# Optimization experiments

Measured on AMD Instinct MI355X. Metric: run time of the kernel, lower is better.

Reference implementation:

```python
import jax, jax.numpy as jnp
import numpy as np

B = 1024        # number of dialogs
MX_LEN = 110    # max utterances per dialog (alpha width hardcoded to 110 in source)
G_DIM = 512     # node feature dim
WP, WF = 10, 10 # past / future window
ALPHA_W = 110
NEG = -1e9


def setup_inputs() -> dict:
    key = jax.random.key(0)
    k1, k2, k3 = jax.random.split(key, 3)
    node_features = jax.random.normal(k1, (B, MX_LEN, G_DIM), dtype=jnp.float32)
    var = 2.0 / (G_DIM + G_DIM)  # matches torch init: normal_(0, var)
    weight = jax.random.normal(k2, (G_DIM, G_DIM), dtype=jnp.float32) * var
    text_len = jax.random.randint(k3, (B,), 1, MX_LEN + 1)
    return {"node_features": node_features, "weight": weight, "text_len": text_len}


def reference(node_features, weight, text_len):
    Bsz, L, D = node_features.shape
    # att_matrix[b, l] = weight @ node_features[b, l]
    att = jnp.einsum('de,ble->bld', weight, node_features)            # [B, L, D]
    # score[b, j, l] = att[b, l] . node_features[b, j]
    scores = jnp.einsum('bld,bjd->bjl', att, node_features)           # [B, J, Lkey]
    j = jnp.arange(L)[:, None]   # query position
    l = jnp.arange(L)[None, :]   # key position
    lens = text_len[:, None, None]                                    # [B, 1, 1]
    # window: s = max(0, j-wp), e = min(j+wf, cur_len-1); valid only for j < cur_len
    mask = (l >= j - WP) & (l <= j + WF) & (l <= lens - 1) & (j <= lens - 1)
    probs = jax.nn.softmax(jnp.where(mask, scores, NEG), axis=-1)
    probs = jnp.where(mask, probs, 0.0)                               # [B, L, L]
    # alpha is [mx_len, 110] per batch, zero outside window; stack over batch
    alpha = jnp.zeros((Bsz, L, ALPHA_W), dtype=probs.dtype).at[:, :, :L].set(probs)
    return alpha
```

## Files before the change

kernel.cpp:

```cpp
#include <hip/hip_runtime.h>
#include <stdint.h>

#define L_SZ 110
#define D_SZ 512
#define OUT_W 110
#define A_STRIDE 520
#define C_STRIDE 136
#define A_ROWS 112
#define ATT_ROWS 112
#define NF_ROWS 112
#define G3_ST 40

typedef __attribute__((ext_vector_type(8))) __bf16 bf16x8;
typedef __attribute__((ext_vector_type(4))) __bf16 bf16x4;
typedef __attribute__((ext_vector_type(4))) float f32x4;

__global__ __launch_bounds__(256) void wconv_kernel(const float* __restrict__ W,
                                                    __bf16* __restrict__ wbf) {
    int idx = blockIdx.x * 256 + threadIdx.x;
    float4 w = ((const float4*)W)[idx];
    bf16x4 o;
    o[0] = (__bf16)w.x; o[1] = (__bf16)w.y; o[2] = (__bf16)w.z; o[3] = (__bf16)w.w;
    ((bf16x4*)wbf)[idx] = o;
}

__global__ __launch_bounds__(256, 5) void att_gemm6_kernel(
    const float* __restrict__ nf, const __bf16* __restrict__ wbf,
    const int* __restrict__ tlenp, __bf16* __restrict__ attws,
    __bf16* __restrict__ nfbf)
{
    __shared__ __bf16 A_lds[64 * G3_ST];
    __shared__ __bf16 B_lds[128 * G3_ST];

    const int b   = blockIdx.y;
    const int cg  = blockIdx.x & 3;
    const int mh  = blockIdx.x >> 2;
    const int tid = threadIdx.x;
    const int lane = tid & 63;
    const int wave = tid >> 6;
    const int l15  = lane & 15;
    const int quad = lane >> 4;

    int len = tlenp[b];
    if (len > L_SZ) len = L_SZ;
    if (len < 1) len = 1;
    const int T = (len + 15) >> 4;
    if (T <= mh * 4) return;
    const int Tl = (T - mh * 4 < 4) ? (T - mh * 4) : 4;
    const int rows_needed = T << 4;
    const int rbase = mh << 6;

    const float* nfb = nf + (size_t)b * (L_SZ * D_SZ);

    const int r0 = tid >> 2;
    const int c8 = (tid & 3) << 3;
    const int ga = rbase + r0;
    const int astat = (ga >= rows_needed) ? 0 : ((ga < L_SZ) ? 1 : 2);

    f32x4 acc[4][2];
    const f32x4 fz = {0.f, 0.f, 0.f, 0.f};
    #pragma unroll
    for (int m = 0; m < 4; ++m) { acc[m][0] = fz; acc[m][1] = fz; }

    float4 abuf[2];
    bf16x8 bbuf[2];

    auto load_tiles = [&](int k0) {
        if (astat == 1) {
            const float* ap = nfb + (size_t)ga * D_SZ + k0 + c8;
            abuf[0] = *(const float4*)ap;
            abuf[1] = *(const float4*)(ap + 4);
        }
        #pragma unroll
        for (int s = 0; s < 2; ++s)
            bbuf[s] = *(const bf16x8*)&wbf[(size_t)(cg * 128 + r0 + 64 * s) * D_SZ + k0 + c8];
    };
    auto store_tiles = [&](int kcur) {
        if (astat) {
            bf16x8 o;
            if (astat == 1) {
                o[0]=(__bf16)abuf[0].x; o[1]=(__bf16)abuf[0].y;
                o[2]=(__bf16)abuf[0].z; o[3]=(__bf16)abuf[0].w;
                o[4]=(__bf16)abuf[1].x; o[5]=(__bf16)abuf[1].y;
                o[6]=(__bf16)abuf[1].z; o[7]=(__bf16)abuf[1].w;
            } else {
                o[0]=o[1]=o[2]=o[3]=o[4]=o[5]=o[6]=o[7]=(__bf16)0.0f;
            }
            *(bf16x8*)&A_lds[r0 * G3_ST + c8] = o;
            if (cg == 0) {
                *(bf16x8*)&nfbf[((size_t)b * NF_ROWS + ga) * D_SZ + kcur + c8] = o;
            }
        }
        #pragma unroll
        for (int s = 0; s < 2; ++s)
            *(bf16x8*)&B_lds[(r0 + 64 * s) * G3_ST + c8] = bbuf[s];
    };

    load_tiles(0);
    for (int kt = 0; kt < 16; ++kt) {
        store_tiles(kt << 5);
        __syncthreads();
        if (kt < 15) load_tiles((kt + 1) << 5);
        bf16x8 bfr[2];
        #pragma unroll
        for (int ni = 0; ni < 2; ++ni)
            bfr[ni] = *(const bf16x8*)&B_lds[(wave * 32 + ni * 16 + l15) * G3_ST + quad * 8];
        #pragma unroll
        for (int m = 0; m < 4; ++m) {
            if (m < Tl) {
                bf16x8 af = *(const bf16x8*)&A_lds[(m * 16 + l15) * G3_ST + quad * 8];
                acc[m][0] = __builtin_amdgcn_mfma_f32_16x16x32_bf16(af, bfr[0], acc[m][0], 0, 0, 0);
                acc[m][1] = __builtin_amdgcn_mfma_f32_16x16x32_bf16(af, bfr[1], acc[m][1], 0, 0, 0);
            }
        }
        __syncthreads();
    }

    __bf16* tw = &A_lds[wave * 16 * G3_ST];
    const size_t obase = (size_t)b * (ATT_ROWS * D_SZ) + cg * 128 + wave * 32;
    const int erow = lane >> 2;
    const int ec8  = (lane & 3) << 3;
    #pragma unroll
    for (int m = 0; m < 4; ++m) {
        if (m < Tl) {
            #pragma unroll
            for (int ni = 0; ni < 2; ++ni)
                #pragma unroll
                for (int r = 0; r < 4; ++r)
                    tw[(quad * 4 + r) * G3_ST + ni * 16 + l15] = (__bf16)acc[m][ni][r];
            bf16x8 v = *(const bf16x8*)&tw[erow * G3_ST + ec8];
            *(bf16x8*)&attws[obase + (size_t)(rbase + m * 16 + erow) * D_SZ + ec8] = v;
        }
    }
}

__global__ __launch_bounds__(256) void band4_kernel(
    const __bf16* __restrict__ nfbf, const __bf16* __restrict__ attws,
    const int* __restrict__ tlenp, float* __restrict__ out)
{
    __shared__ __bf16 KV[64 * D_SZ];
    __shared__ float S[16 * 52];

    const int tj = blockIdx.x;
    const int b  = blockIdx.y;
    const int tid = threadIdx.x;
    const int lane = tid & 63;
    const int wave = tid >> 6;
    const int l15 = lane & 15;
    const int quad = lane >> 4;

    int len = tlenp[b];
    if (len > L_SZ) len = L_SZ;
    if (len < 1) len = 1;
    const int T = (len + 15) >> 4;
    if (tj >= T) return;

    bool tv[3];
    #pragma unroll
    for (int t = 0; t < 3; ++t) {
        int tl = tj - 1 + t;
        tv[t] = (tl >= 0) && (tl < T);
    }

    {
        const int bt = wave - 1;
        const bool do_stage = (wave == 0) || tv[bt];
        if (do_stage) {
            const __bf16* gsrc = (wave == 0)
                ? &nfbf[((size_t)b * NF_ROWS + (tj << 4)) * D_SZ]
                : &attws[((size_t)b * ATT_ROWS + ((tj - 1 + bt) << 4)) * D_SZ];
            __bf16* lbase = &KV[(size_t)(wave * 16) * D_SZ];
            bf16x8 st[16];
            #pragma unroll
            for (int i = 0; i < 16; ++i)
                st[i] = *(const bf16x8*)&gsrc[(size_t)i * D_SZ + (lane << 3)];
            #pragma unroll
            for (int i = 0; i < 16; ++i) {
                int ch = lane ^ (i & 7);
                *(bf16x8*)&lbase[i * D_SZ + (ch << 3)] = st[i];
            }
        }
    }
    __syncthreads();

    if (wave < 3 && tv[wave]) {
        const __bf16* arow = &KV[0];
        const __bf16* brow = &KV[(size_t)((wave + 1) * 16) * D_SZ];
        const f32x4 fz = {0.f, 0.f, 0.f, 0.f};
        f32x4 acc = fz;
        #pragma unroll
        for (int kt = 0; kt < 16; ++kt) {
            int ca = (kt * 4 + quad) ^ (l15 & 7);
            bf16x8 af = *(const bf16x8*)&arow[l15 * D_SZ + (ca << 3)];
            bf16x8 bf = *(const bf16x8*)&brow[l15 * D_SZ + (ca << 3)];
            acc = __builtin_amdgcn_mfma_f32_16x16x32_bf16(af, bf, acc, 0, 0, 0);
        }
        #pragma unroll
        for (int r = 0; r < 4; ++r)
            S[(quad * 4 + r) * 52 + wave * 16 + l15] = acc[r];
    }
    __syncthreads();

    const int srow = tid >> 4;
    const int sc   = tid & 15;
    const int j = (tj << 4) + srow;
    float* outb = out + (size_t)b * (L_SZ * OUT_W);

    float v[3]; bool mk[3];
    float vmax = -3.0e38f;
    #pragma unroll
    for (int t = 0; t < 3; ++t) {
        int tl = tj - 1 + t;
        int l = (tl << 4) + sc;
        bool in = tv[t] && (j < len) && (l < len)
                  && (l >= j - 10) && (l <= j + 10);
        float val = in ? S[srow * 52 + t * 16 + sc] : -3.0e38f;
        mk[t] = in; v[t] = val;
        vmax = fmaxf(vmax, val);
    }
    #pragma unroll
    for (int s = 1; s < 16; s <<= 1)
        vmax = fmaxf(vmax, __shfl_xor(vmax, s, 16));
    float e[3]; float esum = 0.f;
    #pragma unroll
    for (int t = 0; t < 3; ++t) {
        e[t] = mk[t] ? __expf(v[t] - vmax) : 0.f;
        esum += e[t];
    }
    #pragma unroll
    for (int s = 1; s < 16; s <<= 1)
        esum += __shfl_xor(esum, s, 16);
    float inv = (esum > 0.f) ? (1.0f / esum) : 0.f;
    if (j < OUT_W) {
        #pragma unroll
        for (int t = 0; t < 3; ++t) {
            if (tv[t]) {
                int l = ((tj - 1 + t) << 4) + sc;
                if (l < OUT_W) outb[(size_t)j * OUT_W + l] = e[t] * inv;
            }
        }
    }
}

__global__ __launch_bounds__(256, 3) void att_gemm3_kernel(
    const float* __restrict__ nf, const __bf16* __restrict__ wbf,
    const int* __restrict__ tlenp, __bf16* __restrict__ attws)
{
    __shared__ __bf16 A_lds[112 * G3_ST];
    __shared__ __bf16 B_lds[128 * G3_ST];

    const int b   = blockIdx.y;
    const int cg  = blockIdx.x;
    const int tid = threadIdx.x;
    const int lane = tid & 63;
    const int wave = tid >> 6;
    const int l15  = lane & 15;
    const int quad = lane >> 4;

    int len = tlenp[b];
    if (len > L_SZ) len = L_SZ;
    if (len < 1) len = 1;
    const int T = (len + 15) >> 4;
    const int rows_needed = T << 4;

    const float* nfb = nf + (size_t)b * (L_SZ * D_SZ);

    const int r0 = tid >> 2;
    const int c8 = (tid & 3) << 3;
    const int rows2[2] = { r0, r0 + 64 };
    int stat[2];
    #pragma unroll
    for (int s = 0; s < 2; ++s) {
        int r = rows2[s];
        stat[s] = (r >= rows_needed) ? 0 : ((r < L_SZ) ? 1 : 2);
    }

    f32x4 acc[7][2];
    const f32x4 fz = {0.f, 0.f, 0.f, 0.f};
    #pragma unroll
    for (int m = 0; m < 7; ++m) { acc[m][0] = fz; acc[m][1] = fz; }

    float4 abuf[2][2];
    bf16x8 bbuf[2];

    auto load_tiles = [&](int k0) {
        #pragma unroll
        for (int s = 0; s < 2; ++s) {
            if (stat[s] == 1) {
                const float* ap = nfb + (size_t)rows2[s] * D_SZ + k0 + c8;
                abuf[s][0] = *(const float4*)ap;
                abuf[s][1] = *(const float4*)(ap + 4);
            }
            bbuf[s] = *(const bf16x8*)&wbf[(size_t)(cg * 128 + rows2[s]) * D_SZ + k0 + c8];
        }
    };
    auto store_tiles = [&]() {
        #pragma unroll
        for (int s = 0; s < 2; ++s) {
            if (stat[s]) {
                bf16x8 o;
                if (stat[s] == 1) {
                    o[0]=(__bf16)abuf[s][0].x; o[1]=(__bf16)abuf[s][0].y;
                    o[2]=(__bf16)abuf[s][0].z; o[3]=(__bf16)abuf[s][0].w;
                    o[4]=(__bf16)abuf[s][1].x; o[5]=(__bf16)abuf[s][1].y;
                    o[6]=(__bf16)abuf[s][1].z; o[7]=(__bf16)abuf[s][1].w;
                } else {
                    o[0]=o[1]=o[2]=o[3]=o[4]=o[5]=o[6]=o[7]=(__bf16)0.0f;
                }
                *(bf16x8*)&A_lds[rows2[s] * G3_ST + c8] = o;
            }
            *(bf16x8*)&B_lds[rows2[s] * G3_ST + c8] = bbuf[s];
        }
    };

    load_tiles(0);
    for (int kt = 0; kt < 16; ++kt) {
        store_tiles();
        __syncthreads();
        if (kt < 15) load_tiles((kt + 1) << 5);
        bf16x8 bfr[2];
        #pragma unroll
        for (int ni = 0; ni < 2; ++ni)
            bfr[ni] = *(const bf16x8*)&B_lds[(wave * 32 + ni * 16 + l15) * G3_ST + quad * 8];
        #pragma unroll
        for (int m = 0; m < 7; ++m) {
            if (m < T) {
                bf16x8 af = *(const bf16x8*)&A_lds[(m * 16 + l15) * G3_ST + quad * 8];
                acc[m][0] = __builtin_amdgcn_mfma_f32_16x16x32_bf16(af, bfr[0], acc[m][0], 0, 0, 0);
                acc[m][1] = __builtin_amdgcn_mfma_f32_16x16x32_bf16(af, bfr[1], acc[m][1], 0, 0, 0);
            }
        }
        __syncthreads();
    }

    __bf16* tw = &A_lds[wave * 16 * G3_ST];
    const size_t obase = (size_t)b * (ATT_ROWS * D_SZ) + cg * 128 + wave * 32;
    const int erow = lane >> 2;
    const int ec8  = (lane & 3) << 3;
    #pragma unroll
    for (int m = 0; m < 7; ++m) {
        if (m < T) {
            #pragma unroll
            for (int ni = 0; ni < 2; ++ni)
                #pragma unroll
                for (int r = 0; r < 4; ++r)
                    tw[(quad * 4 + r) * G3_ST + ni * 16 + l15] = (__bf16)acc[m][ni][r];
            bf16x8 v = *(const bf16x8*)&tw[erow * G3_ST + ec8];
            *(bf16x8*)&attws[obase + (size_t)(m * 16 + erow) * D_SZ + ec8] = v;
        }
    }
}

__global__ __launch_bounds__(256) void band_kernel(
    const float* __restrict__ nf, const __bf16* __restrict__ attws,
    const int* __restrict__ tlenp, float* __restrict__ out)
{
    const int b = blockIdx.x;
    const int tid = threadIdx.x;
    const int lane = tid & 63;
    const int wave = tid >> 6;
    const int l15 = lane & 15;
    const int quad = lane >> 4;

    int len = tlenp[b];
    if (len > L_SZ) len = L_SZ;
    if (len < 1) len = 1;
    const int T = (len + 15) >> 4;

    const float* nfb = nf + (size_t)b * (L_SZ * D_SZ);
    float* outb = out + (size_t)b * (L_SZ * OUT_W);

    const f32x4 fz = {0.f, 0.f, 0.f, 0.f};
    f32x4 accS[2][3];
    #pragma unroll
    for (int i = 0; i < 2; ++i)
        #pragma unroll
        for (int t = 0; t < 3; ++t) accS[i][t] = fz;

    #pragma unroll
    for (int i = 0; i < 2; ++i) {
        const int tj = wave + (i << 2);
        if (tj < T) {
            int jr = (tj << 4) + l15;
            if (jr > L_SZ - 1) jr = L_SZ - 1;
            const float* ap0 = &nfb[(size_t)jr * D_SZ];
            for (int k0 = 0; k0 < D_SZ; k0 += 32) {
                float4 a0 = *(const float4*)(ap0 + k0 + (quad << 3));
                float4 a1 = *(const float4*)(ap0 + k0 + (quad << 3) + 4);
                bf16x8 af;
                af[0] = (__bf16)a0.x; af[1] = (__bf16)a0.y;
                af[2] = (__bf16)a0.z; af[3] = (__bf16)a0.w;
                af[4] = (__bf16)a1.x; af[5] = (__bf16)a1.y;
                af[6] = (__bf16)a1.z; af[7] = (__bf16)a1.w;
                #pragma unroll
                for (int t = 0; t < 3; ++t) {
                    int tl = tj - 1 + t;
                    if (tl >= 0 && tl < T) {
                        bf16x8 bfr = *(const bf16x8*)&attws[((size_t)b * ATT_ROWS + (tl << 4) + l15) * D_SZ + k0 + (quad << 3)];
                        accS[i][t] = __builtin_amdgcn_mfma_f32_16x16x32_bf16(
                            af, bfr, accS[i][t], 0, 0, 0);
                    }
                }
            }
        }
    }

    #pragma unroll
    for (int i = 0; i < 2; ++i) {
        int tj = wave + 4 * i;
        if (tj >= T) continue;
        #pragma unroll
        for (int r = 0; r < 4; ++r) {
            int j = tj * 16 + quad * 4 + r;
            float v[3]; bool mk[3];
            float vmax = -3.0e38f;
            #pragma unroll
            for (int t = 0; t < 3; ++t) {
                int tl = tj - 1 + t;
                int l = tl * 16 + l15;
                bool in = (tl >= 0) && (tl < T) && (j < len) && (l < len)
                          && (l >= j - 10) && (l <= j + 10);
                float val = in ? accS[i][t][r] : -3.0e38f;
                mk[t] = in; v[t] = val;
                vmax = fmaxf(vmax, val);
            }
            #pragma unroll
            for (int s = 1; s < 16; s <<= 1)
                vmax = fmaxf(vmax, __shfl_xor(vmax, s, 16));
            float e[3]; float esum = 0.f;
            #pragma unroll
            for (int t = 0; t < 3; ++t) {
                e[t] = mk[t] ? __expf(v[t] - vmax) : 0.f;
                esum += e[t];
            }
            #pragma unroll
            for (int s = 1; s < 16; s <<= 1)
                esum += __shfl_xor(esum, s, 16);
            float inv = (esum > 0.f) ? (1.0f / esum) : 0.f;
            if (j < OUT_W) {
                #pragma unroll
                for (int t = 0; t < 3; ++t) {
                    int tl = tj - 1 + t;
                    if (tl >= 0 && tl < T) {
                        int l = tl * 16 + l15;
                        if (l < OUT_W) outb[(size_t)j * OUT_W + l] = e[t] * inv;
                    }
                }
            }
        }
    }
}

__global__ __launch_bounds__(256, 1) void edgeatt_kernel(
    const float* __restrict__ nf, const float* __restrict__ Wf,
    const __bf16* __restrict__ wbf, const int* __restrict__ tlenp,
    float* __restrict__ out, int use_wb)
{
    __shared__ __bf16 A_lds[A_ROWS * A_STRIDE];
    __shared__ __bf16 C_lds[A_ROWS * C_STRIDE];

    const int b = blockIdx.x;
    const int tid = threadIdx.x;
    const int lane = tid & 63;
    const int wave = tid >> 6;
    const int l15 = lane & 15;
    const int quad = lane >> 4;

    int len = tlenp[b];
    if (len > L_SZ) len = L_SZ;
    if (len < 1) len = 1;
    const int T = (len + 15) >> 4;

    const float* nfb = nf + (size_t)b * (L_SZ * D_SZ);
    float* outb = out + (size_t)b * (L_SZ * OUT_W);

    {
        int total4 = len * (D_SZ / 4);
        for (int idx = tid; idx < total4; idx += 256) {
            int row = idx >> 7;
            int c4 = idx & 127;
            float4 v = ((const float4*)nfb)[row * 128 + c4];
            bf16x4 o;
            o[0]=(__bf16)v.x; o[1]=(__bf16)v.y; o[2]=(__bf16)v.z; o[3]=(__bf16)v.w;
            *(bf16x4*)&A_lds[row * A_STRIDE + c4 * 4] = o;
        }
        int zr = 16 * T - len;
        if (zr > 0) {
            int per = A_STRIDE / 4;
            int totalz = zr * per;
            for (int idx = tid; idx < totalz; idx += 256) {
                int row = len + idx / per;
                int c4 = idx % per;
                bf16x4 z; z[0]=z[1]=z[2]=z[3]=(__bf16)0.0f;
                *(bf16x4*)&A_lds[row * A_STRIDE + c4 * 4] = z;
            }
        }
    }
    __syncthreads();

    const int wm = wave >> 1, wn = wave & 1;
    const int h = (T + 1) >> 1;
    const int mt_lo = (wm == 0) ? 0 : h;
    const int nmt = ((wm == 0) ? h : T) - mt_lo;

    const f32x4 fzero = {0.f, 0.f, 0.f, 0.f};
    f32x4 accS[2][3];
    #pragma unroll
    for (int i = 0; i < 2; ++i)
        #pragma unroll
        for (int t = 0; t < 3; ++t) accS[i][t] = fzero;

    for (int c = 0; c < 4; ++c) {
        const int d0 = c * 128;
        f32x4 acc1[4][4];
        #pragma unroll
        for (int mi = 0; mi < 4; ++mi)
            #pragma unroll
            for (int ni = 0; ni < 4; ++ni) acc1[mi][ni] = fzero;

        if (nmt > 0) {
            for (int k0 = 0; k0 < D_SZ; k0 += 32) {
                bf16x8 afrag[4], bfrag[4];
                #pragma unroll
                for (int ni = 0; ni < 4; ++ni) {
                    int d = d0 + (wn * 4 + ni) * 16 + l15;
                    if (use_wb) {
                        bfrag[ni] = *(const bf16x8*)&wbf[(size_t)d * D_SZ + k0 + quad * 8];
                    } else {
                        const float* wp = &Wf[(size_t)d * D_SZ + k0 + quad * 8];
                        float4 w0 = *(const float4*)wp;
                        float4 w1 = *(const float4*)(wp + 4);
                        bf16x8 bb;
                        bb[0]=(__bf16)w0.x; bb[1]=(__bf16)w0.y; bb[2]=(__bf16)w0.z; bb[3]=(__bf16)w0.w;
                        bb[4]=(__bf16)w1.x; bb[5]=(__bf16)w1.y; bb[6]=(__bf16)w1.z; bb[7]=(__bf16)w1.w;
                        bfrag[ni] = bb;
                    }
                }
                #pragma unroll
                for (int mi = 0; mi < 4; ++mi) {
                    if (mi < nmt) {
                        int row = (mt_lo + mi) * 16 + l15;
                        afrag[mi] = *(const bf16x8*)&A_lds[row * A_STRIDE + k0 + quad * 8];
                    }
                }
                #pragma unroll
                for (int mi = 0; mi < 4; ++mi) {
                    if (mi < nmt) {
                        #pragma unroll
                        for (int ni = 0; ni < 4; ++ni)
                            acc1[mi][ni] = __builtin_amdgcn_mfma_f32_16x16x32_bf16(
                                afrag[mi], bfrag[ni], acc1[mi][ni], 0, 0, 0);
                    }
                }
            }
        }
        __syncthreads();

        #pragma unroll
        for (int mi = 0; mi < 4; ++mi) {
            if (mi < nmt) {
                int lbase = (mt_lo + mi) * 16 + quad * 4;
                #pragma unroll
                for (int ni = 0; ni < 4; ++ni) {
                    int dloc = (wn * 4 + ni) * 16 + l15;
                    #pragma unroll
                    for (int r = 0; r < 4; ++r)
                        C_lds[(lbase + r) * C_STRIDE + dloc] = (__bf16)acc1[mi][ni][r];
                }
            }
        }
        __syncthreads();

        for (int kk = 0; kk < 128; kk += 32) {
            #pragma unroll
            for (int i = 0; i < 2; ++i) {
                int tj = wave + 4 * i;
                if (tj < T) {
                    bf16x8 aj = *(const bf16x8*)&A_lds[(tj * 16 + l15) * A_STRIDE + d0 + kk + quad * 8];
                    #pragma unroll
                    for (int t = 0; t < 3; ++t) {
                        int tl = tj - 1 + t;
                        if (tl >= 0 && tl < T) {
                            bf16x8 bj = *(const bf16x8*)&C_lds[(tl * 16 + l15) * C_STRIDE + kk + quad * 8];
                            accS[i][t] = __builtin_amdgcn_mfma_f32_16x16x32_bf16(
                                aj, bj, accS[i][t], 0, 0, 0);
                        }
                    }
                }
            }
        }
        __syncthreads();
    }

    #pragma unroll
    for (int i = 0; i < 2; ++i) {
        int tj = wave + 4 * i;
        if (tj >= T) continue;
        #pragma unroll
        for (int r = 0; r < 4; ++r) {
            int j = tj * 16 + quad * 4 + r;
            float v[3]; bool mk[3];
            float vmax = -3.0e38f;
            #pragma unroll
            for (int t = 0; t < 3; ++t) {
                int tl = tj - 1 + t;
                int l = tl * 16 + l15;
                bool in = (tl >= 0) && (tl < T) && (j < len) && (l < len)
                          && (l >= j - 10) && (l <= j + 10);
                float val = in ? accS[i][t][r] : -3.0e38f;
                mk[t] = in; v[t] = val;
                vmax = fmaxf(vmax, val);
            }
            #pragma unroll
            for (int s = 1; s < 16; s <<= 1)
                vmax = fmaxf(vmax, __shfl_xor(vmax, s, 16));
            float e[3]; float esum = 0.f;
            #pragma unroll
            for (int t = 0; t < 3; ++t) {
                e[t] = mk[t] ? __expf(v[t] - vmax) : 0.f;
                esum += e[t];
            }
            #pragma unroll
            for (int s = 1; s < 16; s <<= 1)
                esum += __shfl_xor(esum, s, 16);
            float inv = (esum > 0.f) ? (1.0f / esum) : 0.f;
            if (j < OUT_W) {
                #pragma unroll
                for (int t = 0; t < 3; ++t) {
                    int tl = tj - 1 + t;
                    if (tl >= 0 && tl < T) {
                        int l = tl * 16 + l15;
                        if (l < OUT_W) outb[(size_t)j * OUT_W + l] = e[t] * inv;
                    }
                }
            }
        }
    }
}

extern "C" void kernel_launch(void* const* d_in, const int* in_sizes, int n_in,
                              void* d_out, int out_size, void* d_ws, size_t ws_size,
                              hipStream_t stream) {
    const float* nf = (const float*)d_in[0];
    const float* W  = (const float*)d_in[1];
    const int* tl   = (const int*)d_in[2];
    float* out      = (float*)d_out;
    __bf16* wbf     = (__bf16*)d_ws;
    const int B = in_sizes[2];

    const size_t wb_bytes  = (size_t)D_SZ * D_SZ * sizeof(__bf16);
    const size_t att_bytes = (size_t)B * ATT_ROWS * D_SZ * sizeof(__bf16);
    const size_t nf_bytes  = (size_t)B * NF_ROWS * D_SZ * sizeof(__bf16);
    const int use_wb = (ws_size >= wb_bytes) ? 1 : 0;
    const int fast   = (use_wb && ws_size >= wb_bytes + att_bytes) ? 1 : 0;
    const int fast2  = (fast && ws_size >= wb_bytes + att_bytes + nf_bytes) ? 1 : 0;

    hipMemsetAsync(d_out, 0, (size_t)out_size * sizeof(float), stream);

    if (use_wb) {
        hipLaunchKernelGGL(wconv_kernel, dim3(256), dim3(256), 0, stream, W, wbf);
    }
    if (fast2) {
        __bf16* attws = (__bf16*)((char*)d_ws + wb_bytes);
        __bf16* nfbf  = (__bf16*)((char*)d_ws + wb_bytes + att_bytes);
        hipLaunchKernelGGL(att_gemm6_kernel, dim3(8, B), dim3(256), 0, stream, nf, wbf, tl, attws, nfbf);
        hipLaunchKernelGGL(band4_kernel, dim3(7, B), dim3(256), 0, stream, nfbf, attws, tl, out);
    } else if (fast) {
        __bf16* attws = (__bf16*)((char*)d_ws + wb_bytes);
        hipLaunchKernelGGL(att_gemm3_kernel, dim3(4, B), dim3(256), 0, stream, nf, wbf, tl, attws);
        hipLaunchKernelGGL(band_kernel, dim3(B), dim3(256), 0, stream, nf, attws, tl, out);
    } else {
        hipLaunchKernelGGL(edgeatt_kernel, dim3(B), dim3(256), 0, stream,
                           nf, W, wbf, tl, out, use_wb);
    }
}
```

Baseline: 494.9 us.

## Cover full 112-row M tile per GEMM block with K=64 steps and XCD-aware block swizzle

The attention GEMM now has each block compute all up to 7 row tiles for one 128-column group, where before two M-halves ran in separate blocks. It also doubles the K step to 64 so there are half as many barriers, and remaps linear block IDs so consecutive work spreads across the 8 XCDs. This removes the duplicated weight-tile loads across M halves and cuts sync overhead. The cost is more LDS and registers per block (occupancy hint drops from 5 to 3) and a larger serial workload per block. The band kernel gets the same 1D swizzled grid mapping.

New measurement: 401.6 us. 18.9% less time.

```diff
diff --git a/kernel.cpp b/kernel.cpp
--- a/kernel.cpp
+++ b/kernel.cpp
@@ -10,6 +10,7 @@
 #define ATT_ROWS 112
 #define NF_ROWS 112
 #define G3_ST 40
+#define G7_ST 72
 
 typedef __attribute__((ext_vector_type(8))) __bf16 bf16x8;
 typedef __attribute__((ext_vector_type(4))) __bf16 bf16x4;
@@ -24,17 +25,20 @@
     ((bf16x4*)wbf)[idx] = o;
 }
 
-__global__ __launch_bounds__(256, 5) void att_gemm6_kernel(
+__global__ __launch_bounds__(256, 3) void att_gemm7_kernel(
     const float* __restrict__ nf, const __bf16* __restrict__ wbf,
     const int* __restrict__ tlenp, __bf16* __restrict__ attws,
     __bf16* __restrict__ nfbf)
 {
-    __shared__ __bf16 A_lds[64 * G3_ST];
-    __shared__ __bf16 B_lds[128 * G3_ST];
-
-    const int b   = blockIdx.y;
-    const int cg  = blockIdx.x & 3;
-    const int mh  = blockIdx.x >> 2;
+    __shared__ __bf16 A_lds[112 * G7_ST];
+    __shared__ __bf16 B_lds[128 * G7_ST];
+
+    const int gid   = blockIdx.x;
+    const int total = gridDim.x;
+    const int w = ((total & 7) == 0) ? ((gid & 7) * (total >> 3) + (gid >> 3)) : gid;
+    const int b  = w >> 2;
+    const int cg = w & 3;
+
     const int tid = threadIdx.x;
     const int lane = tid & 63;
     const int wave = tid >> 6;
@@ -45,72 +49,80 @@
     if (len > L_SZ) len = L_SZ;
     if (len < 1) len = 1;
     const int T = (len + 15) >> 4;
-    if (T <= mh * 4) return;
-    const int Tl = (T - mh * 4 < 4) ? (T - mh * 4) : 4;
     const int rows_needed = T << 4;
-    const int rbase = mh << 6;
 
     const float* nfb = nf + (size_t)b * (L_SZ * D_SZ);
 
-    const int r0 = tid >> 2;
-    const int c8 = (tid & 3) << 3;
-    const int ga = rbase + r0;
-    const int astat = (ga >= rows_needed) ? 0 : ((ga < L_SZ) ? 1 : 2);
-
-    f32x4 acc[4][2];
+    const int rowg = tid >> 3;
+    const int c8   = (tid & 7) << 3;
+    int astat[4];
+    #pragma unroll
+    for (int s = 0; s < 4; ++s) {
+        int r = rowg + 32 * s;
+        astat[s] = (r >= rows_needed) ? 0 : ((r < L_SZ) ? 1 : 2);
+    }
+
+    f32x4 acc[7][2];
     const f32x4 fz = {0.f, 0.f, 0.f, 0.f};
     #pragma unroll
-    for (int m = 0; m < 4; ++m) { acc[m][0] = fz; acc[m][1] = fz; }
-
-    float4 abuf[2];
-    bf16x8 bbuf[2];
+    for (int m = 0; m < 7; ++m) { acc[m][0] = fz; acc[m][1] = fz; }
+
+    float4 abuf[4][2];
+    bf16x8 bbuf[4];
 
     auto load_tiles = [&](int k0) {
-        if (astat == 1) {
-            const float* ap = nfb + (size_t)ga * D_SZ + k0 + c8;
-            abuf[0] = *(const float4*)ap;
-            abuf[1] = *(const float4*)(ap + 4);
-        }
-        #pragma unroll
-        for (int s = 0; s < 2; ++s)
-            bbuf[s] = *(const bf16x8*)&wbf[(size_t)(cg * 128 + r0 + 64 * s) * D_SZ + k0 + c8];
+        #pragma unroll
+        for (int s = 0; s < 4; ++s) {
+            int r = rowg + 32 * s;
+            if (astat[s] == 1) {
+                const float* ap = nfb + (size_t)r * D_SZ + k0 + c8;
+                abuf[s][0] = *(const float4*)ap;
+                abuf[s][1] = *(const float4*)(ap + 4);
+            }
+            bbuf[s] = *(const bf16x8*)&wbf[(size_t)(cg * 128 + r) * D_SZ + k0 + c8];
+        }
     };
     auto store_tiles = [&](int kcur) {
-        if (astat) {
-            bf16x8 o;
-            if (astat == 1) {
-                o[0]=(__bf16)abuf[0].x; o[1]=(__bf16)abuf[0].y;
-                o[2]=(__bf16)abuf[0].z; o[3]=(__bf16)abuf[0].w;
-                o[4]=(__bf16)abuf[1].x; o[5]=(__bf16)abuf[1].y;
-                o[6]=(__bf16)abuf[1].z; o[7]=(__bf16)abuf[1].w;
-            } else {
-                o[0]=o[1]=o[2]=o[3]=o[4]=o[5]=o[6]=o[7]=(__bf16)0.0f;
-            }
-            *(bf16x8*)&A_lds[r0 * G3_ST + c8] = o;
-            if (cg == 0) {
-                *(bf16x8*)&nfbf[((size_t)b * NF_ROWS + ga) * D_SZ + kcur + c8] = o;
-            }
-        }
-        #pragma unroll
-        for (int s = 0; s < 2; ++s)
-            *(bf16x8*)&B_lds[(r0 + 64 * s) * G3_ST + c8] = bbuf[s];
+        #pragma unroll
+        for (int s = 0; s < 4; ++s) {
+            int r = rowg + 32 * s;
+            if (astat[s]) {
+                bf16x8 o;
+                if (astat[s] == 1) {
+                    o[0]=(__bf16)abuf[s][0].x; o[1]=(__bf16)abuf[s][0].y;
+                    o[2]=(__bf16)abuf[s][0].z; o[3]=(__bf16)abuf[s][0].w;
+                    o[4]=(__bf16)abuf[s][1].x; o[5]=(__bf16)abuf[s][1].y;
+                    o[6]=(__bf16)abuf[s][1].z; o[7]=(__bf16)abuf[s][1].w;
+                } else {
+                    o[0]=o[1]=o[2]=o[3]=o[4]=o[5]=o[6]=o[7]=(__bf16)0.0f;
+                }
+                *(bf16x8*)&A_lds[r * G7_ST + c8] = o;
+                if (cg == 0) {
+                    *(bf16x8*)&nfbf[((size_t)b * NF_ROWS + r) * D_SZ + kcur + c8] = o;
+                }
+            }
+            *(bf16x8*)&B_lds[r * G7_ST + c8] = bbuf[s];
+        }
     };
 
     load_tiles(0);
-    for (int kt = 0; kt < 16; ++kt) {
-        store_tiles(kt << 5);
+    for (int kt = 0; kt < 8; ++kt) {
+        store_tiles(kt << 6);
         __syncthreads();
-        if (kt < 15) load_tiles((kt + 1) << 5);
-        bf16x8 bfr[2];
-        #pragma unroll
-        for (int ni = 0; ni < 2; ++ni)
-            bfr[ni] = *(const bf16x8*)&B_lds[(wave * 32 + ni * 16 + l15) * G3_ST + quad * 8];
-        #pragma unroll
-        for (int m = 0; m < 4; ++m) {
-            if (m < Tl) {
-                bf16x8 af = *(const bf16x8*)&A_lds[(m * 16 + l15) * G3_ST + quad * 8];
-                acc[m][0] = __builtin_amdgcn_mfma_f32_16x16x32_bf16(af, bfr[0], acc[m][0], 0, 0, 0);
-                acc[m][1] = __builtin_amdgcn_mfma_f32_16x16x32_bf16(af, bfr[1], acc[m][1], 0, 0, 0);
+        if (kt < 7) load_tiles((kt + 1) << 6);
+        #pragma unroll
+        for (int kk = 0; kk < 64; kk += 32) {
+            bf16x8 bfr[2];
+            #pragma unroll
+            for (int ni = 0; ni < 2; ++ni)
+                bfr[ni] = *(const bf16x8*)&B_lds[(wave * 32 + ni * 16 + l15) * G7_ST + kk + quad * 8];
+            #pragma unroll
+            for (int m = 0; m < 7; ++m) {
+                if (m < T) {
+                    bf16x8 af = *(const bf16x8*)&A_lds[(m * 16 + l15) * G7_ST + kk + quad * 8];
+                    acc[m][0] = __builtin_amdgcn_mfma_f32_16x16x32_bf16(af, bfr[0], acc[m][0], 0, 0, 0);
+                    acc[m][1] = __builtin_amdgcn_mfma_f32_16x16x32_bf16(af, bfr[1], acc[m][1], 0, 0, 0);
+                }
             }
         }
         __syncthreads();
@@ -121,28 +133,32 @@
     const int erow = lane >> 2;
     const int ec8  = (lane & 3) << 3;
     #pragma unroll
-    for (int m = 0; m < 4; ++m) {
-        if (m < Tl) {
+    for (int m = 0; m < 7; ++m) {
+        if (m < T) {
             #pragma unroll
             for (int ni = 0; ni < 2; ++ni)
                 #pragma unroll
                 for (int r = 0; r < 4; ++r)
                     tw[(quad * 4 + r) * G3_ST + ni * 16 + l15] = (__bf16)acc[m][ni][r];
             bf16x8 v = *(const bf16x8*)&tw[erow * G3_ST + ec8];
-            *(bf16x8*)&attws[obase + (size_t)(rbase + m * 16 + erow) * D_SZ + ec8] = v;
+            *(bf16x8*)&attws[obase + (size_t)(m * 16 + erow) * D_SZ + ec8] = v;
         }
     }
 }
 
-__global__ __launch_bounds__(256) void band4_kernel(
+__global__ __launch_bounds__(256) void band5_kernel(
     const __bf16* __restrict__ nfbf, const __bf16* __restrict__ attws,
     const int* __restrict__ tlenp, float* __restrict__ out)
 {
     __shared__ __bf16 KV[64 * D_SZ];
     __shared__ float S[16 * 52];
 
-    const int tj = blockIdx.x;
-    const int b  = blockIdx.y;
+    const int gid   = blockIdx.x;
+    const int total = gridDim.x;
+    const int wkid = ((total & 7) == 0) ? ((gid & 7) * (total >> 3) + (gid >> 3)) : gid;
+    const int b  = wkid / 7;
+    const int tj = wkid - b * 7;
+
     const int tid = threadIdx.x;
     const int lane = tid & 63;
     const int wave = tid >> 6;
@@ -663,8 +679,8 @@
     if (fast2) {
         __bf16* attws = (__bf16*)((char*)d_ws + wb_bytes);
         __bf16* nfbf  = (__bf16*)((char*)d_ws + wb_bytes + att_bytes);
-        hipLaunchKernelGGL(att_gemm6_kernel, dim3(8, B), dim3(256), 0, stream, nf, wbf, tl, attws, nfbf);
-        hipLaunchKernelGGL(band4_kernel, dim3(7, B), dim3(256), 0, stream, nfbf, attws, tl, out);
+        hipLaunchKernelGGL(att_gemm7_kernel, dim3(4 * B), dim3(256), 0, stream, nf, wbf, tl, attws, nfbf);
+        hipLaunchKernelGGL(band5_kernel, dim3(7 * B), dim3(256), 0, stream, nfbf, attws, tl, out);
     } else if (fast) {
         __bf16* attws = (__bf16*)((char*)d_ws + wb_bytes);
         hipLaunchKernelGGL(att_gemm3_kernel, dim3(4, B), dim3(256), 0, stream, nf, wbf, tl, attws);
```
